# Optimization experiments

Hardware: AMD Instinct MI355X
Metric: run time of the kernel (lower is better)

The kernel has to match this reference:

```python
import jax, jax.numpy as jnp
import numpy as np

N, E = 20000, 200000
HID, NH, L = 128, 8, 7
DH = HID // NH
SCALE = float(np.sqrt(DH))
NNUM = 5
MLP_IN = HID + HID + 8 + 8 + 8 + NNUM  # 285
EPS = 1e-5


def _ln(x, g, b):
    mu = jnp.mean(x, -1, keepdims=True)
    var = jnp.mean((x - mu) ** 2, -1, keepdims=True)
    return (x - mu) * jax.lax.rsqrt(var + EPS) * g + b


def setup_inputs() -> dict:
    key = jax.random.key(0)
    ks = jax.random.split(key, 24)
    f = lambda k, s: (0.05 * jax.random.normal(k, s)).astype(jnp.float32)
    z = lambda s: jnp.zeros(s, jnp.float32)
    o = lambda s: jnp.ones(s, jnp.float32)
    inp = {
        'node_feats': f(ks[0], (N, 2)),
        'numericals': f(ks[1], (E, NNUM)),
        'W_emb': f(ks[2], (2, HID)), 'b_emb': z((HID,)),
        'WQ': f(ks[3], (L, HID, HID)), 'bQ': z((L, HID)),
        'WK': f(ks[4], (L, HID, HID)), 'bK': z((L, HID)),
        'WV': f(ks[5], (L, HID, HID)), 'bV': z((L, HID)),
        'WO': f(ks[6], (L, HID, HID)), 'bO': z((L, HID)),
        'ln1_g': o((L, HID)), 'ln1_b': z((L, HID)),
        'ln2_g': o((L, HID)), 'ln2_b': z((L, HID)),
        'W1': f(ks[7], (L, HID, HID)), 'b1': z((L, HID)),
        'W2': f(ks[8], (L, HID, HID)), 'b2': z((L, HID)),
        'curr_emb': f(ks[9], (15, 8)), 'pay_emb': f(ks[10], (7, 8)),
        'mlp_Wh': f(ks[11], (3, MLP_IN, MLP_IN)), 'mlp_bh': z((3, MLP_IN)),
        'mlp_Wo': f(ks[12], (MLP_IN, 2)), 'mlp_bo': z((2,)),
        'src': jax.random.randint(ks[13], (E,), 0, N, dtype=jnp.int32),
        'dst': jax.random.randint(ks[14], (E,), 0, N, dtype=jnp.int32),
        'payment_currency': jax.random.randint(ks[15], (E,), 0, 15, dtype=jnp.int32),
        'receiving_currency': jax.random.randint(ks[16], (E,), 0, 15, dtype=jnp.int32),
        'payment_format': jax.random.randint(ks[17], (E,), 0, 7, dtype=jnp.int32),
    }
    return inp


def reference(node_feats, numericals, W_emb, b_emb, WQ, bQ, WK, bK, WV, bV, WO, bO,
              ln1_g, ln1_b, ln2_g, ln2_b, W1, b1, W2, b2, curr_emb, pay_emb,
              mlp_Wh, mlp_bh, mlp_Wo, mlp_bo, src, dst,
              payment_currency, receiving_currency, payment_format):
    h = node_feats @ W_emb + b_emb  # [N, HID]
    for l in range(L):
        # --- graph multi-head attention (segment softmax over in-edges of dst) ---
        x = _ln(h, ln1_g[l], ln1_b[l])
        Q = (x @ WQ[l] + bQ[l]).reshape(N, NH, DH)
        K = (x @ WK[l] + bK[l]).reshape(N, NH, DH)
        V = (x @ WV[l] + bV[l]).reshape(N, NH, DH)
        scores = jnp.einsum('ehd,ehd->eh', Q[dst], K[src]) / SCALE  # [E, NH]
        m = jax.ops.segment_max(scores, dst, num_segments=N)        # [N, NH]
        ex = jnp.exp(scores - m[dst])
        den = jax.ops.segment_sum(ex, dst, num_segments=N)
        w = ex / den[dst]                                           # attn weights per edge
        attn = jax.ops.segment_sum(w[:, :, None] * V[src], dst, num_segments=N)
        h = h + attn.reshape(N, HID) @ WO[l] + bO[l]
        # --- FFN ---
        x = _ln(h, ln2_g[l], ln2_b[l])
        h = h + jax.nn.relu(x @ W1[l] + b1[l]) @ W2[l] + b2[l]
    # --- edge classifier ---
    ef = jnp.concatenate([curr_emb[payment_currency], curr_emb[receiving_currency],
                          pay_emb[payment_format], numericals], axis=1)  # [E, 29]
    y = jnp.concatenate([h[src], h[dst], ef], axis=1)  # [E, 285]
    for i in range(3):
        y = jax.nn.relu(y @ mlp_Wh[i] + mlp_bh[i])
    return y @ mlp_Wo + mlp_bo  # [E, 2]
```

## Files before the change

kernel.cpp:

```cpp
#include <hip/hip_runtime.h>

#define HID 128
#define NH 8
#define DH 16
#define NLAYERS 7
#define MLP_IN 285
#define MP 288
#define LDW 296
#define XS 136

typedef short short8 __attribute__((ext_vector_type(8)));
typedef float f32x4 __attribute__((ext_vector_type(4)));
typedef float f32x16 __attribute__((ext_vector_type(16)));
typedef unsigned short ushort8 __attribute__((ext_vector_type(8)));

__device__ inline unsigned short f2bf(float f) {
    union { float f; unsigned int u; } v; v.f = f;
    unsigned int r = v.u + 0x7FFF + ((v.u >> 16) & 1);
    return (unsigned short)(r >> 16);
}
__device__ inline float bf2f(unsigned short u) {
    union { unsigned int u; float f; } v; v.u = ((unsigned int)u) << 16;
    return v.f;
}

__global__ __launch_bounds__(256) void embed_kernel(
    const float* __restrict__ nf, const float* __restrict__ We,
    const float* __restrict__ be, float* __restrict__ h, int N)
{
    int idx = blockIdx.x * 256 + threadIdx.x;
    if (idx >= N * HID) return;
    int n = idx >> 7, j = idx & 127;
    h[idx] = fmaf(nf[n * 2], We[j], fmaf(nf[n * 2 + 1], We[HID + j], be[j]));
}

__global__ __launch_bounds__(256) void prep_nodew_kernel(
    const float* __restrict__ WQ, const float* __restrict__ WK,
    const float* __restrict__ WV, const float* __restrict__ WO,
    const float* __restrict__ W1, const float* __restrict__ W2,
    unsigned short* __restrict__ wnh, unsigned short* __restrict__ wnl)
{
    int idx = blockIdx.x * 256 + threadIdx.x;
    if (idx >= 42 * 32 * 64) return;
    int lane = idx & 63;
    int r = idx >> 6;
    int kt = r & 7; r >>= 3;
    int ct = r & 3; r >>= 2;
    int m = r;
    int l = m / 6, wi = m - l * 6;
    const float* Wb;
    switch (wi) {
        case 0: Wb = WQ; break; case 1: Wb = WK; break; case 2: Wb = WV; break;
        case 3: Wb = WO; break; case 4: Wb = W1; break; default: Wb = W2; break;
    }
    Wb += (size_t)l * HID * HID;
    int n = ct * 32 + (lane & 31);
    int kb = kt * 16 + (lane >> 5) * 8;
    ushort8 vh, vl;
#pragma unroll
    for (int j = 0; j < 8; ++j) {
        float w = Wb[(size_t)(kb + j) * HID + n];
        unsigned short hi = f2bf(w);
        vh[j] = hi;
        vl[j] = f2bf(w - bf2f(hi));
    }
    *(ushort8*)&wnh[(size_t)idx * 8] = vh;
    *(ushort8*)&wnl[(size_t)idx * 8] = vl;
}

#define LOADB(m, BH, BL) do { \
    size_t fb_ = (((size_t)(matbase + (m)) * 32 + (size_t)wave * 8) * 64 + lane) * 8; \
    const unsigned short* Bh_ = wnh + fb_; \
    const unsigned short* Bl_ = wnl + fb_; \
    _Pragma("unroll") \
    for (int kt = 0; kt < 8; ++kt) { \
        BH[kt] = *(const short8*)&Bh_[kt * 512]; \
        BL[kt] = *(const short8*)&Bl_[kt * 512]; \
    } \
} while (0)

#define COMPSTORE(BH, BL, BIAS, OUT, STRIDE, OFF) do { \
    f32x16 acc = {}; \
    _Pragma("unroll") \
    for (int kt = 0; kt < 8; ++kt) \
        acc = __builtin_amdgcn_mfma_f32_32x32x16_bf16(ah[kt], BH[kt], acc, 0, 0, 0); \
    _Pragma("unroll") \
    for (int kt = 0; kt < 8; ++kt) \
        acc = __builtin_amdgcn_mfma_f32_32x32x16_bf16(al[kt], BH[kt], acc, 0, 0, 0); \
    _Pragma("unroll") \
    for (int kt = 0; kt < 8; ++kt) \
        acc = __builtin_amdgcn_mfma_f32_32x32x16_bf16(ah[kt], BL[kt], acc, 0, 0, 0); \
    int col_ = wave * 32 + l31; \
    float bv_ = (BIAS)[col_]; \
    _Pragma("unroll") \
    for (int r = 0; r < 16; ++r) { \
        int rowm_ = (r & 3) + 8 * (r >> 2) + 4 * half; \
        int row_ = rowBase + rowm_; \
        if (row_ < M) (OUT)[(size_t)row_ * (STRIDE) + (OFF) + col_] = acc[r] + bv_; \
    } \
} while (0)

__global__ __launch_bounds__(256, 2) void ln_qkv_mfma(
    const float* __restrict__ h,
    const float* __restrict__ g, const float* __restrict__ bb,
    const unsigned short* __restrict__ wnh, const unsigned short* __restrict__ wnl,
    int matbase,
    const float* __restrict__ bQ, const float* __restrict__ bK, const float* __restrict__ bV,
    float* __restrict__ qo, float* __restrict__ kvo, int M)
{
    __shared__ unsigned short Xh[32][XS];
    __shared__ unsigned short Xl[32][XS];
    int tid = threadIdx.x;
    int lane = tid & 63, wave = tid >> 6;
    int rowBase = blockIdx.x * 32;

    for (int i = 0; i < 8; ++i) {
        int r = wave * 8 + i;
        int row = rowBase + r;
        float a0 = 0.f, a1 = 0.f;
        if (row < M) {
            a0 = h[(size_t)row * HID + lane];
            a1 = h[(size_t)row * HID + 64 + lane];
        }
        float s = a0 + a1;
#pragma unroll
        for (int off = 32; off > 0; off >>= 1) s += __shfl_down(s, off, 64);
        s = __shfl(s, 0, 64);
        float mu = s * (1.0f / 128.0f);
        float d0 = a0 - mu, d1 = a1 - mu;
        float v = d0 * d0 + d1 * d1;
#pragma unroll
        for (int off = 32; off > 0; off >>= 1) v += __shfl_down(v, off, 64);
        v = __shfl(v, 0, 64);
        float rr = rsqrtf(v * (1.0f / 128.0f) + 1e-5f);
        float x0 = d0 * rr * g[lane] + bb[lane];
        float x1 = d1 * rr * g[64 + lane] + bb[64 + lane];
        unsigned short h0 = f2bf(x0), h1 = f2bf(x1);
        Xh[r][lane] = h0;           Xh[r][64 + lane] = h1;
        Xl[r][lane] = f2bf(x0 - bf2f(h0));
        Xl[r][64 + lane] = f2bf(x1 - bf2f(h1));
    }
    __syncthreads();

    int l31 = lane & 31;
    int half = lane >> 5;

    short8 ah[8], al[8];
#pragma unroll
    for (int kt = 0; kt < 8; ++kt) {
        ah[kt] = *(const short8*)&Xh[l31][kt * 16 + half * 8];
        al[kt] = *(const short8*)&Xl[l31][kt * 16 + half * 8];
    }

    short8 bh0[8], bl0[8], bh1[8], bl1[8];
    LOADB(0, bh0, bl0);
    LOADB(1, bh1, bl1);
    COMPSTORE(bh0, bl0, bQ, qo, HID, 0);
    LOADB(2, bh0, bl0);
    COMPSTORE(bh1, bl1, bK, kvo, 256, 0);
    COMPSTORE(bh0, bl0, bV, kvo, 256, 128);
}

__global__ __launch_bounds__(256, 2) void post_mfma(
    const float* __restrict__ at, const float* __restrict__ hin,
    const unsigned short* __restrict__ wnh, const unsigned short* __restrict__ wnl,
    int matbase,
    const float* __restrict__ bO,
    const float* __restrict__ g2, const float* __restrict__ b2g,
    const float* __restrict__ b1, const float* __restrict__ b2,
    float* __restrict__ hout, int M)
{
    __shared__ unsigned short Ah[32][XS];
    __shared__ unsigned short Al[32][XS];
    __shared__ unsigned short Th[32][XS];
    __shared__ unsigned short Tl[32][XS];
    __shared__ float Hs[32][132];
    int tid = threadIdx.x;
    int lane = tid & 63, wave = tid >> 6;
    int rowBase = blockIdx.x * 32;
    int l31 = lane & 31;
    int half = lane >> 5;

    for (int i = tid; i < 32 * 32; i += 256) {
        int r = i >> 5, c4 = i & 31;
        int row = rowBase + r;
        float4 va = make_float4(0.f, 0.f, 0.f, 0.f), vh = va;
        if (row < M) {
            va = *(const float4*)&at[(size_t)row * HID + c4 * 4];
            vh = *(const float4*)&hin[(size_t)row * HID + c4 * 4];
        }
        const float* vp = (const float*)&va;
#pragma unroll
        for (int q = 0; q < 4; ++q) {
            unsigned short hi = f2bf(vp[q]);
            Ah[r][c4 * 4 + q] = hi;
            Al[r][c4 * 4 + q] = f2bf(vp[q] - bf2f(hi));
        }
        *(float4*)&Hs[r][c4 * 4] = vh;
    }
    __syncthreads();

    int colW = wave * 32 + l31;

    {
        short8 ah[8], al[8];
#pragma unroll
        for (int kt = 0; kt < 8; ++kt) {
            ah[kt] = *(const short8*)&Ah[l31][kt * 16 + half * 8];
            al[kt] = *(const short8*)&Al[l31][kt * 16 + half * 8];
        }
        short8 bh[8], bl[8];
        {
            size_t fb = (((size_t)(matbase + 3) * 32 + (size_t)wave * 8) * 64 + lane) * 8;
            const unsigned short* Bh = wnh + fb;
            const unsigned short* Bl = wnl + fb;
#pragma unroll
            for (int kt = 0; kt < 8; ++kt) {
                bh[kt] = *(const short8*)&Bh[kt * 512];
                bl[kt] = *(const short8*)&Bl[kt * 512];
            }
        }
        f32x16 acc = {};
#pragma unroll
        for (int kt = 0; kt < 8; ++kt)
            acc = __builtin_amdgcn_mfma_f32_32x32x16_bf16(ah[kt], bh[kt], acc, 0, 0, 0);
#pragma unroll
        for (int kt = 0; kt < 8; ++kt)
            acc = __builtin_amdgcn_mfma_f32_32x32x16_bf16(al[kt], bh[kt], acc, 0, 0, 0);
#pragma unroll
        for (int kt = 0; kt < 8; ++kt)
            acc = __builtin_amdgcn_mfma_f32_32x32x16_bf16(ah[kt], bl[kt], acc, 0, 0, 0);
        float bv = bO[colW];
#pragma unroll
        for (int r = 0; r < 16; ++r) {
            int rowm = (r & 3) + 8 * (r >> 2) + 4 * half;
            Hs[rowm][colW] += acc[r] + bv;
        }
    }
    __syncthreads();

    for (int i = 0; i < 8; ++i) {
        int r = wave * 8 + i;
        float a0 = Hs[r][lane];
        float a1 = Hs[r][64 + lane];
        float s = a0 + a1;
#pragma unroll
        for (int off = 32; off > 0; off >>= 1) s += __shfl_down(s, off, 64);
        s = __shfl(s, 0, 64);
        float mu = s * (1.0f / 128.0f);
        float d0 = a0 - mu, d1 = a1 - mu;
        float v = d0 * d0 + d1 * d1;
#pragma unroll
        for (int off = 32; off > 0; off >>= 1) v += __shfl_down(v, off, 64);
        v = __shfl(v, 0, 64);
        float rr = rsqrtf(v * (1.0f / 128.0f) + 1e-5f);
        float x0 = d0 * rr * g2[lane] + b2g[lane];
        float x1 = d1 * rr * g2[64 + lane] + b2g[64 + lane];
        unsigned short h0 = f2bf(x0), h1 = f2bf(x1);
        Ah[r][lane] = h0;           Ah[r][64 + lane] = h1;
        Al[r][lane] = f2bf(x0 - bf2f(h0));
        Al[r][64 + lane] = f2bf(x1 - bf2f(h1));
    }
    __syncthreads();

    {
        short8 ah[8], al[8];
#pragma unroll
        for (int kt = 0; kt < 8; ++kt) {
            ah[kt] = *(const short8*)&Ah[l31][kt * 16 + half * 8];
            al[kt] = *(const short8*)&Al[l31][kt * 16 + half * 8];
        }
        short8 bh[8], bl[8];
        {
            size_t fb = (((size_t)(matbase + 4) * 32 + (size_t)wave * 8) * 64 + lane) * 8;
            const unsigned short* Bh = wnh + fb;
            const unsigned short* Bl = wnl + fb;
#pragma unroll
            for (int kt = 0; kt < 8; ++kt) {
                bh[kt] = *(const short8*)&Bh[kt * 512];
                bl[kt] = *(const short8*)&Bl[kt * 512];
            }
        }
        f32x16 acc = {};
#pragma unroll
        for (int kt = 0; kt < 8; ++kt)
            acc = __builtin_amdgcn_mfma_f32_32x32x16_bf16(ah[kt], bh[kt], acc, 0, 0, 0);
#pragma unroll
        for (int kt = 0; kt < 8; ++kt)
            acc = __builtin_amdgcn_mfma_f32_32x32x16_bf16(al[kt], bh[kt], acc, 0, 0, 0);
#pragma unroll
        for (int kt = 0; kt < 8; ++kt)
            acc = __builtin_amdgcn_mfma_f32_32x32x16_bf16(ah[kt], bl[kt], acc, 0, 0, 0);
        float bv = b1[colW];
#pragma unroll
        for (int r = 0; r < 16; ++r) {
            int rowm = (r & 3) + 8 * (r >> 2) + 4 * half;
            float t = fmaxf(acc[r] + bv, 0.f);
            unsigned short hi = f2bf(t);
            Th[rowm][colW] = hi;
            Tl[rowm][colW] = f2bf(t - bf2f(hi));
        }
    }
    __syncthreads();

    {
        short8 ah[8], al[8];
#pragma unroll
        for (int kt = 0; kt < 8; ++kt) {
            ah[kt] = *(const short8*)&Th[l31][kt * 16 + half * 8];
            al[kt] = *(const short8*)&Tl[l31][kt * 16 + half * 8];
        }
        short8 bh[8], bl[8];
        {
            size_t fb = (((size_t)(matbase + 5) * 32 + (size_t)wave * 8) * 64 + lane) * 8;
            const unsigned short* Bh = wnh + fb;
            const unsigned short* Bl = wnl + fb;
#pragma unroll
            for (int kt = 0; kt < 8; ++kt) {
                bh[kt] = *(const short8*)&Bh[kt * 512];
                bl[kt] = *(const short8*)&Bl[kt * 512];
            }
        }
        f32x16 acc = {};
#pragma unroll
        for (int kt = 0; kt < 8; ++kt)
            acc = __builtin_amdgcn_mfma_f32_32x32x16_bf16(ah[kt], bh[kt], acc, 0, 0, 0);
#pragma unroll
        for (int kt = 0; kt < 8; ++kt)
            acc = __builtin_amdgcn_mfma_f32_32x32x16_bf16(al[kt], bh[kt], acc, 0, 0, 0);
#pragma unroll
        for (int kt = 0; kt < 8; ++kt)
            acc = __builtin_amdgcn_mfma_f32_32x32x16_bf16(ah[kt], bl[kt], acc, 0, 0, 0);
        float bv = b2[colW];
#pragma unroll
        for (int r = 0; r < 16; ++r) {
            int rowm = (r & 3) + 8 * (r >> 2) + 4 * half;
            int row = rowBase + rowm;
            if (row < M)
                hout[(size_t)row * HID + colW] = Hs[rowm][colW] + acc[r] + bv;
        }
    }
}

__global__ __launch_bounds__(256) void deg_kernel(
    const int* __restrict__ dst, int* __restrict__ deg, int E)
{
    int e = blockIdx.x * 256 + threadIdx.x;
    if (e < E) atomicAdd(&deg[dst[e]], 1);
}

__global__ __launch_bounds__(256) void scan_kernel(
    const int* __restrict__ deg, int* __restrict__ rowptr,
    int* __restrict__ cursor, int N)
{
    __shared__ int sums[256];
    int tid = threadIdx.x;
    int chunk = (N + 255) / 256;
    int lo = tid * chunk;
    int hi = lo + chunk; if (hi > N) hi = N;
    int s = 0;
    for (int i = lo; i < hi && i >= 0; ++i) s += deg[i];
    sums[tid] = s;
    __syncthreads();
    for (int off = 1; off < 256; off <<= 1) {
        int v = (tid >= off) ? sums[tid - off] : 0;
        __syncthreads();
        sums[tid] += v;
        __syncthreads();
    }
    int base = (tid == 0) ? 0 : sums[tid - 1];
    for (int i = lo; i < hi; ++i) {
        rowptr[i] = base; cursor[i] = base; base += deg[i];
    }
    if (tid == 255) rowptr[N] = sums[255];
}

__global__ __launch_bounds__(256) void scatter_kernel(
    const int* __restrict__ src, const int* __restrict__ dst,
    int* __restrict__ cursor, int* __restrict__ ssrc, int E)
{
    int e = blockIdx.x * 256 + threadIdx.x;
    if (e < E) {
        int p = atomicAdd(&cursor[dst[e]], 1);
        ssrc[p] = src[e];
    }
}

__global__ __launch_bounds__(256) void attn_fused_kernel(
    const float* __restrict__ q, const float* __restrict__ kv,
    const int* __restrict__ rowptr, const int* __restrict__ ssrc,
    float* __restrict__ at, int N)
{
    int node = blockIdx.x * 4 + (threadIdx.x >> 6);
    int lane = threadIdx.x & 63;
    if (node >= N) return;
    int beg = rowptr[node], end = rowptr[node + 1];
    float q0 = q[(size_t)node * HID + lane];
    float q1 = q[(size_t)node * HID + 64 + lane];
    float acc0 = 0.f, acc1 = 0.f, den0 = 0.f, den1 = 0.f;
    int i = beg;
    for (; i + 2 <= end; i += 2) {
        int s0 = ssrc[i], s1 = ssrc[i + 1];
        const float* kv0 = kv + (size_t)s0 * 256;
        const float* kv1 = kv + (size_t)s1 * 256;
        float k00 = kv0[lane],       k01 = kv0[64 + lane];
        float v00 = kv0[128 + lane], v01 = kv0[192 + lane];
        float k10 = kv1[lane],       k11 = kv1[64 + lane];
        float v10 = kv1[128 + lane], v11 = kv1[192 + lane];
        float p00 = q0 * k00, p01 = q1 * k01;
        float p10 = q0 * k10, p11 = q1 * k11;
#pragma unroll
        for (int off = 1; off < 16; off <<= 1) {
            p00 += __shfl_xor(p00, off, 64);
            p01 += __shfl_xor(p01, off, 64);
            p10 += __shfl_xor(p10, off, 64);
            p11 += __shfl_xor(p11, off, 64);
        }
        float w00 = __expf(p00 * 0.25f), w01 = __expf(p01 * 0.25f);
        float w10 = __expf(p10 * 0.25f), w11 = __expf(p11 * 0.25f);
        den0 += w00 + w10; den1 += w01 + w11;
        acc0 = fmaf(w10, v10, fmaf(w00, v00, acc0));
        acc1 = fmaf(w11, v11, fmaf(w01, v01, acc1));
    }
    if (i < end) {
        int s = ssrc[i];
        const float* kv0 = kv + (size_t)s * 256;
        float k0 = kv0[lane], k1 = kv0[64 + lane];
        float p0 = q0 * k0, p1 = q1 * k1;
#pragma unroll
        for (int off = 1; off < 16; off <<= 1) {
            p0 += __shfl_xor(p0, off, 64);
            p1 += __shfl_xor(p1, off, 64);
        }
        float w0 = __expf(p0 * 0.25f), w1 = __expf(p1 * 0.25f);
        den0 += w0; den1 += w1;
        acc0 = fmaf(w0, kv0[128 + lane], acc0);
        acc1 = fmaf(w1, kv0[192 + lane], acc1);
    }
    at[(size_t)node * HID + lane]      = (den0 > 0.f) ? acc0 / den0 : 0.f;
    at[(size_t)node * HID + 64 + lane] = (den1 > 0.f) ? acc1 / den1 : 0.f;
}

__global__ __launch_bounds__(256) void prep_wp_kernel(
    const float* __restrict__ Wh, unsigned short* __restrict__ wp)
{
    int idx = blockIdx.x * 256 + threadIdx.x;
    if (idx >= 3 * 9 * 18 * 64) return;
    int lane = idx & 63;
    int r = idx >> 6;
    int kt = r % 18; r /= 18;
    int ct = r % 9;
    int layer = r / 9;
    int n = ct * 32 + (lane & 31);
    int kbase = kt * 16 + (lane >> 5) * 8;
    ushort8 val;
#pragma unroll
    for (int j = 0; j < 8; ++j) {
        int k = kbase + j;
        float v = (n < MLP_IN && k < MLP_IN)
            ? Wh[(size_t)layer * MLP_IN * MLP_IN + (size_t)k * MLP_IN + n] : 0.f;
        val[j] = f2bf(v);
    }
    *(ushort8*)&wp[(size_t)idx * 8] = val;
}

__global__ __launch_bounds__(256) void prep_hb_kernel(
    const float* __restrict__ h, unsigned short* __restrict__ hb, int n)
{
    int idx = blockIdx.x * 256 + threadIdx.x;
    if (idx >= n) return;
    hb[idx] = f2bf(h[idx]);
}

#define ELOADB(ct, BUF) do { \
    const unsigned short* Wp_ = Wb + (size_t)(ct) * 9216; \
    _Pragma("unroll") \
    for (int kt = 0; kt < 18; ++kt) BUF[kt] = *(const short8*)&Wp_[kt * 512]; \
} while (0)

#define EMFMA(ct, BUF) do { \
    f32x16 acc = {}; \
    _Pragma("unroll") \
    for (int kt = 0; kt < 18; ++kt) \
        acc = __builtin_amdgcn_mfma_f32_32x32x16_bf16(afr[kt], BUF[kt], acc, 0, 0, 0); \
    int col_ = (ct) * 32 + l31; \
    if (col_ < MLP_IN) { \
        float bv_ = bias[col_]; \
        _Pragma("unroll") \
        for (int r = 0; r < 16; ++r) { \
            int rowm_ = (r & 3) + 8 * (r >> 2) + 4 * half; \
            y[(wave * 32 + rowm_) * LDW + col_] = f2bf(fmaxf(acc[r] + bv_, 0.f)); \
        } \
    } \
} while (0)

__global__ __launch_bounds__(256, 2) void edge_mlp_mfma(
    const unsigned short* __restrict__ hb, const float* __restrict__ ce,
    const float* __restrict__ pe, const float* __restrict__ num,
    const int* __restrict__ src, const int* __restrict__ dst,
    const int* __restrict__ pc, const int* __restrict__ rc,
    const int* __restrict__ pf,
    const unsigned short* __restrict__ wp, const float* __restrict__ bh,
    const float* __restrict__ Wo, const float* __restrict__ bo,
    float* __restrict__ out, int E)
{
    __shared__ unsigned short y[128 * LDW];
    int tid = threadIdx.x;
    int e0 = blockIdx.x * 128;

    for (int i = tid; i < 128 * 36; i += 256) {
        int t = i / 36;
        int c = i - t * 36;
        int e = e0 + t;
        if (e >= E) e = E - 1;
        ushort8 val;
        if (c < 16) {
            val = *(const ushort8*)&hb[(size_t)src[e] * HID + c * 8];
        } else if (c < 32) {
            val = *(const ushort8*)&hb[(size_t)dst[e] * HID + (c - 16) * 8];
        } else if (c == 32) {
            const float* p = &ce[pc[e] * 8];
#pragma unroll
            for (int j = 0; j < 8; ++j) val[j] = f2bf(p[j]);
        } else if (c == 33) {
            const float* p = &ce[rc[e] * 8];
#pragma unroll
            for (int j = 0; j < 8; ++j) val[j] = f2bf(p[j]);
        } else if (c == 34) {
            const float* p = &pe[pf[e] * 8];
#pragma unroll
            for (int j = 0; j < 8; ++j) val[j] = f2bf(p[j]);
        } else {
            const float* p = &num[(size_t)e * 5];
#pragma unroll
            for (int j = 0; j < 5; ++j) val[j] = f2bf(p[j]);
            val[5] = 0; val[6] = 0; val[7] = 0;
        }
        *(ushort8*)&y[t * LDW + c * 8] = val;
    }
    __syncthreads();

    int wave = tid >> 6;
    int lane = tid & 63;
    int l31 = lane & 31;
    int half = lane >> 5;
    int rowA = wave * 32 + l31;

    for (int layer = 0; layer < 3; ++layer) {
        const unsigned short* __restrict__ Wl = wp + (size_t)layer * 9 * 18 * 64 * 8;
        const float* __restrict__ bias = bh + layer * MLP_IN;
        const unsigned short* Wb = Wl + (size_t)lane * 8;

        short8 afr[18];
#pragma unroll
        for (int kt = 0; kt < 18; ++kt)
            afr[kt] = *(const short8*)&y[rowA * LDW + kt * 16 + half * 8];
        __syncthreads();

        short8 bA[18], bB[18];
        ELOADB(0, bA);
#pragma unroll
        for (int cp = 0; cp < 4; ++cp) {
            ELOADB(cp * 2 + 1, bB);
            EMFMA(cp * 2, bA);
            ELOADB(cp * 2 + 2, bA);
            EMFMA(cp * 2 + 1, bB);
        }
        EMFMA(8, bA);
        __syncthreads();
    }

    {
        int t = tid >> 1, oc = tid & 1;
        int e = e0 + t;
        if (e < E) {
            const unsigned short* yr = &y[t * LDW];
            float p0 = 0.f, p1 = 0.f, p2 = 0.f, p3 = 0.f;
            for (int kc = 0; kc < 35; ++kc) {
                ushort8 yv = *(const ushort8*)&yr[kc * 8];
                int kb = kc * 8;
                p0 = fmaf(bf2f(yv[0]), Wo[(kb + 0) * 2 + oc], p0);
                p1 = fmaf(bf2f(yv[1]), Wo[(kb + 1) * 2 + oc], p1);
                p2 = fmaf(bf2f(yv[2]), Wo[(kb + 2) * 2 + oc], p2);
                p3 = fmaf(bf2f(yv[3]), Wo[(kb + 3) * 2 + oc], p3);
                p0 = fmaf(bf2f(yv[4]), Wo[(kb + 4) * 2 + oc], p0);
                p1 = fmaf(bf2f(yv[5]), Wo[(kb + 5) * 2 + oc], p1);
                p2 = fmaf(bf2f(yv[6]), Wo[(kb + 6) * 2 + oc], p2);
                p3 = fmaf(bf2f(yv[7]), Wo[(kb + 7) * 2 + oc], p3);
            }
            float acc = bo[oc] + (p0 + p1) + (p2 + p3);
            for (int k = 280; k < MLP_IN; ++k)
                acc = fmaf(bf2f(yr[k]), Wo[k * 2 + oc], acc);
            out[(size_t)e * 2 + oc] = acc;
        }
    }
}

extern "C" void kernel_launch(void* const* d_in, const int* in_sizes, int n_in,
                              void* d_out, int out_size, void* d_ws, size_t ws_size,
                              hipStream_t stream)
{
    const float* node_feats = (const float*)d_in[0];
    const float* numericals = (const float*)d_in[1];
    const float* W_emb = (const float*)d_in[2];
    const float* b_emb = (const float*)d_in[3];
    const float* WQ = (const float*)d_in[4];
    const float* bQ = (const float*)d_in[5];
    const float* WK = (const float*)d_in[6];
    const float* bK = (const float*)d_in[7];
    const float* WV = (const float*)d_in[8];
    const float* bV = (const float*)d_in[9];
    const float* WO = (const float*)d_in[10];
    const float* bO = (const float*)d_in[11];
    const float* ln1_g = (const float*)d_in[12];
    const float* ln1_b = (const float*)d_in[13];
    const float* ln2_g = (const float*)d_in[14];
    const float* ln2_b = (const float*)d_in[15];
    const float* W1 = (const float*)d_in[16];
    const float* b1 = (const float*)d_in[17];
    const float* W2 = (const float*)d_in[18];
    const float* b2 = (const float*)d_in[19];
    const float* curr_emb = (const float*)d_in[20];
    const float* pay_emb = (const float*)d_in[21];
    const float* mlp_Wh = (const float*)d_in[22];
    const float* mlp_bh = (const float*)d_in[23];
    const float* mlp_Wo = (const float*)d_in[24];
    const float* mlp_bo = (const float*)d_in[25];
    const int* src = (const int*)d_in[26];
    const int* dst = (const int*)d_in[27];
    const int* pc = (const int*)d_in[28];
    const int* rc = (const int*)d_in[29];
    const int* pf = (const int*)d_in[30];

    const int N = in_sizes[0] / 2;
    const int E = in_sizes[26];

    float* ws = (float*)d_ws;
    float* h   = ws;
    float* qb  = h   + (size_t)N * HID;
    float* kvb = qb  + (size_t)N * HID;
    float* at  = kvb + (size_t)N * HID * 2;
    unsigned short* hb = (unsigned short*)(at + (size_t)N * HID);
    unsigned short* wpk = hb + (size_t)N * HID;
    unsigned short* wnh = wpk + (size_t)3 * 9 * 18 * 64 * 8;
    unsigned short* wnl = wnh + (size_t)42 * 32 * 64 * 8;
    int* rowptr = (int*)(wnl + (size_t)42 * 32 * 64 * 8);
    int* deg    = rowptr + (N + 1);
    int* cursor = deg + N;
    int* ssrc   = cursor + N;

    prep_wp_kernel<<<(3 * 9 * 18 * 64 + 255) / 256, 256, 0, stream>>>(mlp_Wh, wpk);
    prep_nodew_kernel<<<(42 * 32 * 64 + 255) / 256, 256, 0, stream>>>(
        WQ, WK, WV, WO, W1, W2, wnh, wnl);

    embed_kernel<<<(N * HID + 255) / 256, 256, 0, stream>>>(node_feats, W_emb, b_emb, h, N);

    hipMemsetAsync(deg, 0, (size_t)N * sizeof(int), stream);
    deg_kernel<<<(E + 255) / 256, 256, 0, stream>>>(dst, deg, E);
    scan_kernel<<<1, 256, 0, stream>>>(deg, rowptr, cursor, N);
    scatter_kernel<<<(E + 255) / 256, 256, 0, stream>>>(src, dst, cursor, ssrc, E);

    int nodeBlocks = (N + 31) / 32;

    for (int l = 0; l < NLAYERS; ++l) {
        ln_qkv_mfma<<<nodeBlocks, 256, 0, stream>>>(
            h, ln1_g + l * HID, ln1_b + l * HID,
            wnh, wnl, l * 6,
            bQ + l * HID, bK + l * HID, bV + l * HID,
            qb, kvb, N);

        attn_fused_kernel<<<(N + 3) / 4, 256, 0, stream>>>(qb, kvb, rowptr, ssrc, at, N);

        post_mfma<<<nodeBlocks, 256, 0, stream>>>(
            at, h, wnh, wnl, l * 6,
            bO + l * HID,
            ln2_g + l * HID, ln2_b + l * HID,
            b1 + l * HID, b2 + l * HID,
            h, N);
    }

    prep_hb_kernel<<<(N * HID + 255) / 256, 256, 0, stream>>>(h, hb, N * HID);

    edge_mlp_mfma<<<(E + 127) / 128, 256, 0, stream>>>(
        hb, curr_emb, pay_emb, numericals, src, dst, pc, rc, pf,
        wpk, mlp_bh, mlp_Wo, mlp_bo, (float*)d_out, E);
}
```

Baseline: 1.047 ms.

## Restructure edge MLP: 512 threads, column-stationary weights, double-buffered activations

The edge MLP kernel now launches 512 threads per block, and each of the 8 waves keeps one 32-column weight tile resident in registers while it loops over the 4 row tiles. Previously each wave owned 32 rows and streamed all 9 weight column tiles. The ninth column tile is handled by two waves, and the next layer's weights are prefetched before the barrier. Activations ping-pong between two LDS buffers, which removes one barrier per layer, and the output projection is split across two threads joined by a shuffle. The costs are doubled LDS use (about 150 KB per block), A fragments re-read from LDS for every row tile, and load imbalance from the extra column tile.

Measured after the change: 1.079 ms. 1.03x slower.

```diff
diff --git a/kernel.cpp b/kernel.cpp
--- a/kernel.cpp
+++ b/kernel.cpp
@@ -472,29 +472,7 @@
     hb[idx] = f2bf(h[idx]);
 }
 
-#define ELOADB(ct, BUF) do { \
-    const unsigned short* Wp_ = Wb + (size_t)(ct) * 9216; \
-    _Pragma("unroll") \
-    for (int kt = 0; kt < 18; ++kt) BUF[kt] = *(const short8*)&Wp_[kt * 512]; \
-} while (0)
-
-#define EMFMA(ct, BUF) do { \
-    f32x16 acc = {}; \
-    _Pragma("unroll") \
-    for (int kt = 0; kt < 18; ++kt) \
-        acc = __builtin_amdgcn_mfma_f32_32x32x16_bf16(afr[kt], BUF[kt], acc, 0, 0, 0); \
-    int col_ = (ct) * 32 + l31; \
-    if (col_ < MLP_IN) { \
-        float bv_ = bias[col_]; \
-        _Pragma("unroll") \
-        for (int r = 0; r < 16; ++r) { \
-            int rowm_ = (r & 3) + 8 * (r >> 2) + 4 * half; \
-            y[(wave * 32 + rowm_) * LDW + col_] = f2bf(fmaxf(acc[r] + bv_, 0.f)); \
-        } \
-    } \
-} while (0)
-
-__global__ __launch_bounds__(256, 2) void edge_mlp_mfma(
+__global__ __launch_bounds__(512, 2) void edge_mlp_mfma(
     const unsigned short* __restrict__ hb, const float* __restrict__ ce,
     const float* __restrict__ pe, const float* __restrict__ num,
     const int* __restrict__ src, const int* __restrict__ dst,
@@ -504,11 +482,22 @@
     const float* __restrict__ Wo, const float* __restrict__ bo,
     float* __restrict__ out, int E)
 {
-    __shared__ unsigned short y[128 * LDW];
+    __shared__ unsigned short y[2][128 * LDW];
     int tid = threadIdx.x;
     int e0 = blockIdx.x * 128;
-
-    for (int i = tid; i < 128 * 36; i += 256) {
+    int wave = tid >> 6;
+    int lane = tid & 63;
+    int l31 = lane & 31;
+    int half = lane >> 5;
+
+    short8 bb[18];
+    {
+        const unsigned short* Bp = wp + (size_t)wave * 9216 + (size_t)lane * 8;
+#pragma unroll
+        for (int kt = 0; kt < 18; ++kt) bb[kt] = *(const short8*)&Bp[kt * 512];
+    }
+
+    for (int i = tid; i < 128 * 36; i += 512) {
         int t = i / 36;
         int c = i - t * 36;
         int e = e0 + t;
@@ -536,63 +525,119 @@
             for (int j = 0; j < 5; ++j) val[j] = f2bf(p[j]);
             val[5] = 0; val[6] = 0; val[7] = 0;
         }
-        *(ushort8*)&y[t * LDW + c * 8] = val;
+        *(ushort8*)&y[0][t * LDW + c * 8] = val;
+    }
+    for (int rr = tid; rr < 128; rr += 512) {
+        y[1][rr * LDW + 285] = 0;
+        y[1][rr * LDW + 286] = 0;
+        y[1][rr * LDW + 287] = 0;
     }
     __syncthreads();
 
-    int wave = tid >> 6;
-    int lane = tid & 63;
-    int l31 = lane & 31;
-    int half = lane >> 5;
-    int rowA = wave * 32 + l31;
-
     for (int layer = 0; layer < 3; ++layer) {
-        const unsigned short* __restrict__ Wl = wp + (size_t)layer * 9 * 18 * 64 * 8;
+        const unsigned short* __restrict__ yin = y[layer & 1];
+        unsigned short* __restrict__ yout = y[(layer & 1) ^ 1];
         const float* __restrict__ bias = bh + layer * MLP_IN;
-        const unsigned short* Wb = Wl + (size_t)lane * 8;
-
-        short8 afr[18];
-#pragma unroll
-        for (int kt = 0; kt < 18; ++kt)
-            afr[kt] = *(const short8*)&y[rowA * LDW + kt * 16 + half * 8];
+
+        float bvA = bias[wave * 32 + l31];
+
+#pragma unroll
+        for (int rt = 0; rt < 4; ++rt) {
+            short8 afr[18];
+            const unsigned short* ar = &yin[(rt * 32 + l31) * LDW + half * 8];
+#pragma unroll
+            for (int kt = 0; kt < 18; ++kt)
+                afr[kt] = *(const short8*)&ar[kt * 16];
+            f32x16 acc = {};
+#pragma unroll
+            for (int kt = 0; kt < 18; ++kt)
+                acc = __builtin_amdgcn_mfma_f32_32x32x16_bf16(afr[kt], bb[kt], acc, 0, 0, 0);
+            unsigned short* yo = &yout[(size_t)(rt * 32 + 4 * half) * LDW + wave * 32 + l31];
+#pragma unroll
+            for (int j = 0; j < 8; ++j) {
+                float v0 = fmaxf(acc[2 * j] + bvA, 0.f);
+                float v1 = fmaxf(acc[2 * j + 1] + bvA, 0.f);
+                unsigned pk;
+                asm("v_cvt_pk_bf16_f32 %0, %1, %2" : "=v"(pk) : "v"(v0), "v"(v1));
+                int r0 = 2 * j;
+                int rm0 = (r0 & 3) + 8 * (r0 >> 2);
+                yo[rm0 * LDW] = (unsigned short)pk;
+                yo[(rm0 + 1) * LDW] = (unsigned short)(pk >> 16);
+            }
+        }
+
+        if (wave < 2) {
+            const unsigned short* Bp = wp + (size_t)layer * 82944 + (size_t)8 * 9216 + (size_t)lane * 8;
+#pragma unroll
+            for (int kt = 0; kt < 18; ++kt) bb[kt] = *(const short8*)&Bp[kt * 512];
+            int col8 = 256 + l31;
+            float bv8 = (col8 < MLP_IN) ? bias[col8] : 0.f;
+#pragma unroll
+            for (int j8 = 0; j8 < 2; ++j8) {
+                int rt = wave * 2 + j8;
+                short8 afr[18];
+                const unsigned short* ar = &yin[(rt * 32 + l31) * LDW + half * 8];
+#pragma unroll
+                for (int kt = 0; kt < 18; ++kt)
+                    afr[kt] = *(const short8*)&ar[kt * 16];
+                f32x16 acc = {};
+#pragma unroll
+                for (int kt = 0; kt < 18; ++kt)
+                    acc = __builtin_amdgcn_mfma_f32_32x32x16_bf16(afr[kt], bb[kt], acc, 0, 0, 0);
+                if (l31 < 29) {
+                    unsigned short* yo = &yout[(size_t)(rt * 32 + 4 * half) * LDW + col8];
+#pragma unroll
+                    for (int j = 0; j < 8; ++j) {
+                        float v0 = fmaxf(acc[2 * j] + bv8, 0.f);
+                        float v1 = fmaxf(acc[2 * j + 1] + bv8, 0.f);
+                        unsigned pk;
+                        asm("v_cvt_pk_bf16_f32 %0, %1, %2" : "=v"(pk) : "v"(v0), "v"(v1));
+                        int r0 = 2 * j;
+                        int rm0 = (r0 & 3) + 8 * (r0 >> 2);
+                        yo[rm0 * LDW] = (unsigned short)pk;
+                        yo[(rm0 + 1) * LDW] = (unsigned short)(pk >> 16);
+                    }
+                }
+            }
+        }
+
+        if (layer < 2) {
+            const unsigned short* Bp = wp + (size_t)(layer + 1) * 82944 + (size_t)wave * 9216 + (size_t)lane * 8;
+#pragma unroll
+            for (int kt = 0; kt < 18; ++kt) bb[kt] = *(const short8*)&Bp[kt * 512];
+        }
         __syncthreads();
-
-        short8 bA[18], bB[18];
-        ELOADB(0, bA);
-#pragma unroll
-        for (int cp = 0; cp < 4; ++cp) {
-            ELOADB(cp * 2 + 1, bB);
-            EMFMA(cp * 2, bA);
-            ELOADB(cp * 2 + 2, bA);
-            EMFMA(cp * 2 + 1, bB);
-        }
-        EMFMA(8, bA);
-        __syncthreads();
     }
 
     {
-        int t = tid >> 1, oc = tid & 1;
+        int t = tid >> 2;
+        int oc = tid & 1;
+        int kk = (tid >> 1) & 1;
         int e = e0 + t;
-        if (e < E) {
-            const unsigned short* yr = &y[t * LDW];
-            float p0 = 0.f, p1 = 0.f, p2 = 0.f, p3 = 0.f;
-            for (int kc = 0; kc < 35; ++kc) {
-                ushort8 yv = *(const ushort8*)&yr[kc * 8];
-                int kb = kc * 8;
-                p0 = fmaf(bf2f(yv[0]), Wo[(kb + 0) * 2 + oc], p0);
-                p1 = fmaf(bf2f(yv[1]), Wo[(kb + 1) * 2 + oc], p1);
-                p2 = fmaf(bf2f(yv[2]), Wo[(kb + 2) * 2 + oc], p2);
-                p3 = fmaf(bf2f(yv[3]), Wo[(kb + 3) * 2 + oc], p3);
-                p0 = fmaf(bf2f(yv[4]), Wo[(kb + 4) * 2 + oc], p0);
-                p1 = fmaf(bf2f(yv[5]), Wo[(kb + 5) * 2 + oc], p1);
-                p2 = fmaf(bf2f(yv[6]), Wo[(kb + 6) * 2 + oc], p2);
-                p3 = fmaf(bf2f(yv[7]), Wo[(kb + 7) * 2 + oc], p3);
-            }
-            float acc = bo[oc] + (p0 + p1) + (p2 + p3);
+        const unsigned short* yr = &y[1][t * LDW];
+        float p0 = 0.f, p1 = 0.f, p2 = 0.f, p3 = 0.f;
+        int kc_lo = kk ? 18 : 0;
+        int kc_hi = kk ? 35 : 18;
+        for (int kc = kc_lo; kc < kc_hi; ++kc) {
+            ushort8 yv = *(const ushort8*)&yr[kc * 8];
+            int kb = kc * 8;
+            p0 = fmaf(bf2f(yv[0]), Wo[(kb + 0) * 2 + oc], p0);
+            p1 = fmaf(bf2f(yv[1]), Wo[(kb + 1) * 2 + oc], p1);
+            p2 = fmaf(bf2f(yv[2]), Wo[(kb + 2) * 2 + oc], p2);
+            p3 = fmaf(bf2f(yv[3]), Wo[(kb + 3) * 2 + oc], p3);
+            p0 = fmaf(bf2f(yv[4]), Wo[(kb + 4) * 2 + oc], p0);
+            p1 = fmaf(bf2f(yv[5]), Wo[(kb + 5) * 2 + oc], p1);
+            p2 = fmaf(bf2f(yv[6]), Wo[(kb + 6) * 2 + oc], p2);
+            p3 = fmaf(bf2f(yv[7]), Wo[(kb + 7) * 2 + oc], p3);
+        }
+        float acc = (p0 + p1) + (p2 + p3);
+        if (kk) {
             for (int k = 280; k < MLP_IN; ++k)
                 acc = fmaf(bf2f(yr[k]), Wo[k * 2 + oc], acc);
-            out[(size_t)e * 2 + oc] = acc;
-        }
+        }
+        acc += __shfl_xor(acc, 2, 64);
+        if (kk == 0 && e < E)
+            out[(size_t)e * 2 + oc] = acc + bo[oc];
     }
 }
 
@@ -681,7 +726,7 @@
 
     prep_hb_kernel<<<(N * HID + 255) / 256, 256, 0, stream>>>(h, hb, N * HID);
 
-    edge_mlp_mfma<<<(E + 127) / 128, 256, 0, stream>>>(
+    edge_mlp_mfma<<<(E + 127) / 128, 512, 0, stream>>>(
         hb, curr_emb, pay_emb, numericals, src, dst, pc, rc, pf,
         wpk, mlp_bh, mlp_Wo, mlp_bo, (float*)d_out, E);
 }
```

## Split edge MLP column tiles across wave pairs with 64-edge blocks

Applied to the files above, without the earlier changes.

The edge MLP kernel now handles 64 edges per block instead of 128. Each pair of waves shares one 32-row slab, and each wave computes about half of the 9 output column tiles (5 or 4). This halves LDS use per block and raises the occupancy hint from 2 to 4, and the final 285->2 projection is split across two lanes joined with a shuffle. In exchange it drops the double-buffered weight prefetch, so every weight tile is fetched twice as often across blocks, and the per-wave work is unbalanced at 5 versus 4 tiles.

Result: no change. 1.041 ms (-0.5%).

```diff
diff --git a/kernel.cpp b/kernel.cpp
--- a/kernel.cpp
+++ b/kernel.cpp
@@ -472,29 +472,7 @@
     hb[idx] = f2bf(h[idx]);
 }
 
-#define ELOADB(ct, BUF) do { \
-    const unsigned short* Wp_ = Wb + (size_t)(ct) * 9216; \
-    _Pragma("unroll") \
-    for (int kt = 0; kt < 18; ++kt) BUF[kt] = *(const short8*)&Wp_[kt * 512]; \
-} while (0)
-
-#define EMFMA(ct, BUF) do { \
-    f32x16 acc = {}; \
-    _Pragma("unroll") \
-    for (int kt = 0; kt < 18; ++kt) \
-        acc = __builtin_amdgcn_mfma_f32_32x32x16_bf16(afr[kt], BUF[kt], acc, 0, 0, 0); \
-    int col_ = (ct) * 32 + l31; \
-    if (col_ < MLP_IN) { \
-        float bv_ = bias[col_]; \
-        _Pragma("unroll") \
-        for (int r = 0; r < 16; ++r) { \
-            int rowm_ = (r & 3) + 8 * (r >> 2) + 4 * half; \
-            y[(wave * 32 + rowm_) * LDW + col_] = f2bf(fmaxf(acc[r] + bv_, 0.f)); \
-        } \
-    } \
-} while (0)
-
-__global__ __launch_bounds__(256, 2) void edge_mlp_mfma(
+__global__ __launch_bounds__(256, 4) void edge_mlp_mfma(
     const unsigned short* __restrict__ hb, const float* __restrict__ ce,
     const float* __restrict__ pe, const float* __restrict__ num,
     const int* __restrict__ src, const int* __restrict__ dst,
@@ -504,11 +482,15 @@
     const float* __restrict__ Wo, const float* __restrict__ bo,
     float* __restrict__ out, int E)
 {
-    __shared__ unsigned short y[128 * LDW];
+    __shared__ unsigned short y[64 * LDW];
     int tid = threadIdx.x;
-    int e0 = blockIdx.x * 128;
-
-    for (int i = tid; i < 128 * 36; i += 256) {
+    int e0 = blockIdx.x * 64;
+    int wave = tid >> 6;
+    int lane = tid & 63;
+    int l31 = lane & 31;
+    int half = lane >> 5;
+
+    for (int i = tid; i < 64 * 36; i += 256) {
         int t = i / 36;
         int c = i - t * 36;
         int e = e0 + t;
@@ -540,16 +522,13 @@
     }
     __syncthreads();
 
-    int wave = tid >> 6;
-    int lane = tid & 63;
-    int l31 = lane & 31;
-    int half = lane >> 5;
-    int rowA = wave * 32 + l31;
+    int slab = wave >> 1;
+    int rowA = slab * 32 + l31;
+    int ctlo = (wave & 1) ? 5 : 0;
+    int cthi = (wave & 1) ? 9 : 5;
 
     for (int layer = 0; layer < 3; ++layer) {
-        const unsigned short* __restrict__ Wl = wp + (size_t)layer * 9 * 18 * 64 * 8;
         const float* __restrict__ bias = bh + layer * MLP_IN;
-        const unsigned short* Wb = Wl + (size_t)lane * 8;
 
         short8 afr[18];
 #pragma unroll
@@ -557,42 +536,60 @@
             afr[kt] = *(const short8*)&y[rowA * LDW + kt * 16 + half * 8];
         __syncthreads();
 
-        short8 bA[18], bB[18];
-        ELOADB(0, bA);
-#pragma unroll
-        for (int cp = 0; cp < 4; ++cp) {
-            ELOADB(cp * 2 + 1, bB);
-            EMFMA(cp * 2, bA);
-            ELOADB(cp * 2 + 2, bA);
-            EMFMA(cp * 2 + 1, bB);
-        }
-        EMFMA(8, bA);
+        for (int ct = ctlo; ct < cthi; ++ct) {
+            const unsigned short* __restrict__ Bp =
+                wp + (size_t)layer * 82944 + (size_t)ct * 9216 + (size_t)lane * 8;
+            short8 bfr[18];
+#pragma unroll
+            for (int kt = 0; kt < 18; ++kt)
+                bfr[kt] = *(const short8*)&Bp[kt * 512];
+            f32x16 acc = {};
+#pragma unroll
+            for (int kt = 0; kt < 18; ++kt)
+                acc = __builtin_amdgcn_mfma_f32_32x32x16_bf16(afr[kt], bfr[kt], acc, 0, 0, 0);
+            int col = ct * 32 + l31;
+            if (col < MLP_IN) {
+                float bv = bias[col];
+#pragma unroll
+                for (int r = 0; r < 16; ++r) {
+                    int rowm = (r & 3) + 8 * (r >> 2) + 4 * half;
+                    float t = fmaxf(acc[r] + bv, 0.f);
+                    y[(slab * 32 + rowm) * LDW + col] = f2bf(t);
+                }
+            }
+        }
         __syncthreads();
     }
 
     {
-        int t = tid >> 1, oc = tid & 1;
+        int t = tid >> 2;
+        int oc = tid & 1;
+        int kk = (tid >> 1) & 1;
         int e = e0 + t;
-        if (e < E) {
-            const unsigned short* yr = &y[t * LDW];
-            float p0 = 0.f, p1 = 0.f, p2 = 0.f, p3 = 0.f;
-            for (int kc = 0; kc < 35; ++kc) {
-                ushort8 yv = *(const ushort8*)&yr[kc * 8];
-                int kb = kc * 8;
-                p0 = fmaf(bf2f(yv[0]), Wo[(kb + 0) * 2 + oc], p0);
-                p1 = fmaf(bf2f(yv[1]), Wo[(kb + 1) * 2 + oc], p1);
-                p2 = fmaf(bf2f(yv[2]), Wo[(kb + 2) * 2 + oc], p2);
-                p3 = fmaf(bf2f(yv[3]), Wo[(kb + 3) * 2 + oc], p3);
-                p0 = fmaf(bf2f(yv[4]), Wo[(kb + 4) * 2 + oc], p0);
-                p1 = fmaf(bf2f(yv[5]), Wo[(kb + 5) * 2 + oc], p1);
-                p2 = fmaf(bf2f(yv[6]), Wo[(kb + 6) * 2 + oc], p2);
-                p3 = fmaf(bf2f(yv[7]), Wo[(kb + 7) * 2 + oc], p3);
-            }
-            float acc = bo[oc] + (p0 + p1) + (p2 + p3);
+        const unsigned short* yr = &y[t * LDW];
+        float p0 = 0.f, p1 = 0.f, p2 = 0.f, p3 = 0.f;
+        int kc_lo = kk ? 18 : 0;
+        int kc_hi = kk ? 35 : 18;
+        for (int kc = kc_lo; kc < kc_hi; ++kc) {
+            ushort8 yv = *(const ushort8*)&yr[kc * 8];
+            int kb = kc * 8;
+            p0 = fmaf(bf2f(yv[0]), Wo[(kb + 0) * 2 + oc], p0);
+            p1 = fmaf(bf2f(yv[1]), Wo[(kb + 1) * 2 + oc], p1);
+            p2 = fmaf(bf2f(yv[2]), Wo[(kb + 2) * 2 + oc], p2);
+            p3 = fmaf(bf2f(yv[3]), Wo[(kb + 3) * 2 + oc], p3);
+            p0 = fmaf(bf2f(yv[4]), Wo[(kb + 4) * 2 + oc], p0);
+            p1 = fmaf(bf2f(yv[5]), Wo[(kb + 5) * 2 + oc], p1);
+            p2 = fmaf(bf2f(yv[6]), Wo[(kb + 6) * 2 + oc], p2);
+            p3 = fmaf(bf2f(yv[7]), Wo[(kb + 7) * 2 + oc], p3);
+        }
+        float acc = (p0 + p1) + (p2 + p3);
+        if (kk) {
             for (int k = 280; k < MLP_IN; ++k)
                 acc = fmaf(bf2f(yr[k]), Wo[k * 2 + oc], acc);
-            out[(size_t)e * 2 + oc] = acc;
-        }
+        }
+        acc += __shfl_xor(acc, 2, 64);
+        if (kk == 0 && e < E)
+            out[(size_t)e * 2 + oc] = acc + bo[oc];
     }
 }
 
@@ -681,7 +678,7 @@
 
     prep_hb_kernel<<<(N * HID + 255) / 256, 256, 0, stream>>>(h, hb, N * HID);
 
-    edge_mlp_mfma<<<(E + 127) / 128, 256, 0, stream>>>(
+    edge_mlp_mfma<<<(E + 63) / 64, 256, 0, stream>>>(
         hb, curr_emb, pay_emb, numericals, src, dst, pc, rc, pf,
         wpk, mlp_bh, mlp_Wo, mlp_bo, (float*)d_out, E);
 }
```
